# Kernel tuning notes

Hardware: AMD Instinct MI355X
Metric: run time of the kernel (lower is better)

The kernel has to match this reference:

```python
import jax, jax.numpy as jnp
import numpy as np

N = 100000

def _gcn_norm(edge_index, n):
    # PyG GCNConv default: add self-loops, symmetric deg^-1/2 normalization
    loops = jnp.arange(n, dtype=edge_index.dtype)
    src = jnp.concatenate([edge_index[0], loops])
    dst = jnp.concatenate([edge_index[1], loops])
    deg = jax.ops.segment_sum(jnp.ones_like(dst, dtype=jnp.float32), dst, num_segments=n)
    dinv = jnp.where(deg > 0, jax.lax.rsqrt(deg), 0.0)
    norm = dinv[src] * dinv[dst]  # [E+N]
    return src, dst, norm

def _gcn_conv(h, W, b, src, dst, norm, n):
    # transform then gather-scale-scatter aggregate
    h = h @ W                                   # [N, out]
    out = jax.ops.segment_sum(norm[:, None] * h[src], dst, num_segments=n)
    return out + b

def _prelu(h, a):
    return jnp.where(h > 0, h, a * h)

def _dropout(h, u, p=0.5):
    # deterministic dropout: keep where u >= p, scale by 1/(1-p)
    return jnp.where(u >= p, h / (1.0 - p), 0.0)

def setup_inputs() -> dict:
    key = jax.random.key(0)
    ks = jax.random.split(key, 12)
    D, H1, H2, C, E = 512, 128, 16, 10, 1600000
    x = jax.random.normal(ks[0], (N, D), dtype=jnp.float32)
    edge_index = jax.random.randint(ks[1], (2, E), 0, N, dtype=jnp.int64)
    u1 = jax.random.uniform(ks[2], (N, H1), dtype=jnp.float32)
    u2 = jax.random.uniform(ks[3], (N, H2), dtype=jnp.float32)
    def glorot(k, shp):
        lim = np.sqrt(6.0 / (shp[0] + shp[1]))
        return jax.random.uniform(k, shp, dtype=jnp.float32, minval=-lim, maxval=lim)
    W1 = glorot(ks[4], (D, H1)); b1 = jnp.zeros((H1,), jnp.float32)
    W2 = glorot(ks[5], (H1, H2)); b2 = jnp.zeros((H2,), jnp.float32)
    fcW = glorot(ks[6], (H2, C)); fcb = jnp.zeros((C,), jnp.float32)
    a = jnp.float32(0.25)  # PReLU init (shared single param for both layers)
    return {"x": x, "edge_index": edge_index, "W1": W1, "b1": b1, "W2": W2,
            "b2": b2, "a": a, "fcW": fcW, "fcb": fcb, "u1": u1, "u2": u2}

def reference(x, edge_index, W1, b1, W2, b2, a, fcW, fcb, u1, u2):
    src, dst, norm = _gcn_norm(edge_index, N)
    feat1 = _dropout(_prelu(_gcn_conv(x, W1, b1, src, dst, norm, N), a), u1)
    feat2 = _dropout(_prelu(_gcn_conv(feat1, W2, b2, src, dst, norm, N), a), u2)
    logits = feat2 @ fcW + fcb
    return (feat2, logits)
```

## Files before the change

### kernel.cpp

```cpp
#include <hip/hip_runtime.h>
#include <hip/hip_bf16.h>
#include <stdint.h>

#define NN 100000
#define DIN 512
#define H1C 128
#define H2C 16
#define NCLS 10
#define NB_SCAN ((NN + 255) / 256)

typedef __attribute__((ext_vector_type(8))) short s16x8;
typedef __attribute__((ext_vector_type(4))) float f32x4;
typedef __attribute__((ext_vector_type(4))) unsigned short u16x4;
typedef __attribute__((ext_vector_type(8))) unsigned short u16x8;

static __device__ __forceinline__ unsigned short f2bf(float f) {
  __hip_bfloat16 h = __float2bfloat16(f);
  return *(unsigned short*)&h;
}
static __device__ __forceinline__ float bflo(unsigned u) {
  return __uint_as_float(u << 16);
}
static __device__ __forceinline__ float bfhi(unsigned u) {
  return __uint_as_float(u & 0xffff0000u);
}

__device__ __forceinline__ int ld_src(const int* __restrict__ ei, int f, int E, int i) {
  return f ? ei[2 * (size_t)i] : ei[i];
}
__device__ __forceinline__ int ld_dst(const int* __restrict__ ei, int f, int E, int i) {
  return f ? ei[2 * ((size_t)E + (size_t)i)] : ei[(size_t)E + (size_t)i];
}

__global__ void k_pre(const int* __restrict__ ei, int* __restrict__ flag,
                      int* __restrict__ deg,
                      const float* __restrict__ W1, unsigned short* __restrict__ Wt, int n) {
  int i = blockIdx.x * 256 + threadIdx.x;
  if (blockIdx.x == 0 && threadIdx.x < 64) {
    int v = ei[2 * threadIdx.x + 1];
    unsigned long long b = __ballot(v == 0);
    if (threadIdx.x == 0) *flag = (b == ~0ull) ? 1 : 0;
  }
  if (i < n) deg[i] = 0;
  if (i < H1C * DIN) {
    int nn = i >> 9, k = i & 511;
    Wt[i] = f2bf(W1[(size_t)k * H1C + nn]);
  }
}

__global__ void k_count(const int* __restrict__ ei, const int* __restrict__ flag,
                        int E, int* __restrict__ deg, int* __restrict__ rank) {
  int i = blockIdx.x * blockDim.x + threadIdx.x;
  if (i >= E) return;
  int f = *flag;
  rank[i] = atomicAdd(&deg[ld_dst(ei, f, E, i)], 1);
}

__global__ void k_scanA(const int* __restrict__ deg, int* __restrict__ incl,
                        int* __restrict__ bsum, float* __restrict__ dinv, int n) {
  __shared__ int s[256];
  int i = blockIdx.x * 256 + threadIdx.x;
  int v = (i < n) ? deg[i] : 0;
  if (i < n) dinv[i] = rsqrtf((float)(v + 1));
  s[threadIdx.x] = v;
  __syncthreads();
  for (int off = 1; off < 256; off <<= 1) {
    int t = (threadIdx.x >= off) ? s[threadIdx.x - off] : 0;
    __syncthreads();
    s[threadIdx.x] += t;
    __syncthreads();
  }
  if (i < n) incl[i] = s[threadIdx.x];
  if (threadIdx.x == 255) bsum[blockIdx.x] = s[255];
}

__global__ void k_scanB(int* __restrict__ bsum, int nb) {
  __shared__ int s[512];
  int v = (threadIdx.x < nb) ? bsum[threadIdx.x] : 0;
  s[threadIdx.x] = v;
  __syncthreads();
  for (int off = 1; off < 512; off <<= 1) {
    int t = (threadIdx.x >= off) ? s[threadIdx.x - off] : 0;
    __syncthreads();
    s[threadIdx.x] += t;
    __syncthreads();
  }
  if (threadIdx.x < nb) bsum[threadIdx.x] = s[threadIdx.x] - v;
}

__global__ void k_scanC(const int* __restrict__ deg, const int* __restrict__ bsum,
                        int* __restrict__ offs, int n, int E) {
  int i = blockIdx.x * 256 + threadIdx.x;
  if (i < n) offs[i] = offs[i] - deg[i] + bsum[i >> 8];
  if (i == 0) offs[n] = E;
}

__global__ void k_scatter(const int* __restrict__ ei, const int* __restrict__ flag, int E,
                          const int* __restrict__ offs, const int* __restrict__ rank,
                          const float* __restrict__ dinv, uint2* __restrict__ csr_sw) {
  int i = blockIdx.x * blockDim.x + threadIdx.x;
  if (i >= E) return;
  int f = *flag;
  int s = ld_src(ei, f, E, i), d = ld_dst(ei, f, E, i);
  int pos = offs[d] + rank[i];
  uint2 rec;
  rec.x = (unsigned)s;
  rec.y = __float_as_uint(dinv[s]);
  csr_sw[pos] = rec;
}

#define BM 128
#define BK 64
#define LDA 72
#define LDB 72

__global__ __launch_bounds__(256) void k_gemm1_mfma(const float* __restrict__ x,
                                                    const unsigned short* __restrict__ Wt,
                                                    unsigned int* __restrict__ h1u, int n) {
  __shared__ unsigned short As[BM * LDA];
  __shared__ unsigned short Bs[H1C * LDB];
  int tid = threadIdx.x;
  int wave = tid >> 6, lane = tid & 63;
  int wm = wave >> 1, wn = wave & 1;
  int bm = blockIdx.x * BM;
  int lrow = lane & 15, lk = (lane >> 4) * 8;

  f32x4 acc[4][4];
#pragma unroll
  for (int i = 0; i < 4; i++)
#pragma unroll
    for (int j = 0; j < 4; j++) acc[i][j] = (f32x4){0.f, 0.f, 0.f, 0.f};

  for (int k0 = 0; k0 < DIN; k0 += BK) {
#pragma unroll
    for (int p = 0; p < 8; p++) {
      int idx = p * 256 + tid;
      int r = idx >> 4, c4 = (idx & 15) * 4;
      int row = bm + r;
      float4 v = make_float4(0.f, 0.f, 0.f, 0.f);
      if (row < n) v = *(const float4*)(x + (size_t)row * DIN + k0 + c4);
      u16x4 b4;
      b4.x = f2bf(v.x); b4.y = f2bf(v.y); b4.z = f2bf(v.z); b4.w = f2bf(v.w);
      *(u16x4*)&As[r * LDA + c4] = b4;
    }
#pragma unroll
    for (int p = 0; p < 4; p++) {
      int idx = p * 256 + tid;
      int r = idx >> 3, c8 = (idx & 7) * 8;
      int pr = (r & 64) + (((r & 1) + 2 * ((r >> 5) & 1)) << 4) + ((r >> 1) & 15);
      u16x8 v = *(const u16x8*)&Wt[(size_t)r * DIN + k0 + c8];
      *(u16x8*)&Bs[pr * LDB + c8] = v;
    }
    __syncthreads();
#pragma unroll
    for (int kk = 0; kk < 2; kk++) {
      s16x8 a[4], b[4];
#pragma unroll
      for (int mi = 0; mi < 4; mi++)
        a[mi] = *(const s16x8*)&As[(wm * 64 + mi * 16 + lrow) * LDA + kk * 32 + lk];
#pragma unroll
      for (int nj = 0; nj < 4; nj++)
        b[nj] = *(const s16x8*)&Bs[(wn * 64 + nj * 16 + lrow) * LDB + kk * 32 + lk];
#pragma unroll
      for (int mi = 0; mi < 4; mi++)
#pragma unroll
        for (int nj = 0; nj < 4; nj++)
          acc[mi][nj] = __builtin_amdgcn_mfma_f32_16x16x32_bf16(a[mi], b[nj], acc[mi][nj], 0, 0, 0);
    }
    __syncthreads();
  }
#pragma unroll
  for (int mi = 0; mi < 4; mi++) {
#pragma unroll
    for (int r = 0; r < 4; r++) {
      int row = bm + wm * 64 + mi * 16 + (lane >> 4) * 4 + r;
      if (row < n) {
        unsigned p0 = ((unsigned)f2bf(acc[mi][1][r]) << 16) | (unsigned)f2bf(acc[mi][0][r]);
        unsigned p1 = ((unsigned)f2bf(acc[mi][3][r]) << 16) | (unsigned)f2bf(acc[mi][2][r]);
        h1u[(size_t)row * 64 + wn * 32 + lrow] = p0;
        h1u[(size_t)row * 64 + wn * 32 + 16 + lrow] = p1;
      }
    }
  }
}

__global__ __launch_bounds__(256) void k_agg1(const unsigned int* __restrict__ h1u,
                                              const uint2* __restrict__ csr_sw,
                                              const int* __restrict__ offs,
                                              const float* __restrict__ dinv,
                                              const float* __restrict__ b1,
                                              const float* __restrict__ aP,
                                              const float* __restrict__ u1,
                                              unsigned int* __restrict__ f1u, int n) {
  int wid = (blockIdx.x * 256 + threadIdx.x) >> 6;
  int lane = threadIdx.x & 63;
  if (wid >= n) return;
  int d = wid;
  int beg = offs[d], end = offs[d + 1];
  unsigned gs = h1u[(size_t)d * 64 + lane];
  float ax = 0.f, ay = 0.f;
  int e = beg;
  for (; e + 7 < end; e += 8) {
    uint2 r0 = csr_sw[e],     r1 = csr_sw[e + 1], r2 = csr_sw[e + 2], r3 = csr_sw[e + 3];
    uint2 r4 = csr_sw[e + 4], r5 = csr_sw[e + 5], r6 = csr_sw[e + 6], r7 = csr_sw[e + 7];
    unsigned g0 = h1u[(size_t)r0.x * 64 + lane];
    unsigned g1 = h1u[(size_t)r1.x * 64 + lane];
    unsigned g2 = h1u[(size_t)r2.x * 64 + lane];
    unsigned g3 = h1u[(size_t)r3.x * 64 + lane];
    unsigned g4 = h1u[(size_t)r4.x * 64 + lane];
    unsigned g5 = h1u[(size_t)r5.x * 64 + lane];
    unsigned g6 = h1u[(size_t)r6.x * 64 + lane];
    unsigned g7 = h1u[(size_t)r7.x * 64 + lane];
    float w0 = __uint_as_float(r0.y), w1 = __uint_as_float(r1.y);
    float w2 = __uint_as_float(r2.y), w3 = __uint_as_float(r3.y);
    float w4 = __uint_as_float(r4.y), w5 = __uint_as_float(r5.y);
    float w6 = __uint_as_float(r6.y), w7 = __uint_as_float(r7.y);
    ax += w0 * bflo(g0); ay += w0 * bfhi(g0);
    ax += w1 * bflo(g1); ay += w1 * bfhi(g1);
    ax += w2 * bflo(g2); ay += w2 * bfhi(g2);
    ax += w3 * bflo(g3); ay += w3 * bfhi(g3);
    ax += w4 * bflo(g4); ay += w4 * bfhi(g4);
    ax += w5 * bflo(g5); ay += w5 * bfhi(g5);
    ax += w6 * bflo(g6); ay += w6 * bfhi(g6);
    ax += w7 * bflo(g7); ay += w7 * bfhi(g7);
  }
  for (; e + 3 < end; e += 4) {
    uint2 r0 = csr_sw[e], r1 = csr_sw[e + 1], r2 = csr_sw[e + 2], r3 = csr_sw[e + 3];
    unsigned g0 = h1u[(size_t)r0.x * 64 + lane];
    unsigned g1 = h1u[(size_t)r1.x * 64 + lane];
    unsigned g2 = h1u[(size_t)r2.x * 64 + lane];
    unsigned g3 = h1u[(size_t)r3.x * 64 + lane];
    float w0 = __uint_as_float(r0.y), w1 = __uint_as_float(r1.y);
    float w2 = __uint_as_float(r2.y), w3 = __uint_as_float(r3.y);
    ax += w0 * bflo(g0); ay += w0 * bfhi(g0);
    ax += w1 * bflo(g1); ay += w1 * bfhi(g1);
    ax += w2 * bflo(g2); ay += w2 * bfhi(g2);
    ax += w3 * bflo(g3); ay += w3 * bfhi(g3);
  }
  for (; e < end; e++) {
    uint2 rr = csr_sw[e];
    float w = __uint_as_float(rr.y);
    unsigned g = h1u[(size_t)rr.x * 64 + lane];
    ax += w * bflo(g); ay += w * bfhi(g);
  }
  float di = dinv[d];
  ax = (ax + di * bflo(gs)) * di;
  ay = (ay + di * bfhi(gs)) * di;
  float2 bb = ((const float2*)b1)[lane];
  ax += bb.x; ay += bb.y;
  float al = *aP;
  ax = ax > 0.f ? ax : al * ax;
  ay = ay > 0.f ? ay : al * ay;
  float2 uu = ((const float2*)u1)[(size_t)d * 64 + lane];
  ax = (uu.x >= 0.5f) ? ax * 2.f : 0.f;
  ay = (uu.y >= 0.5f) ? ay * 2.f : 0.f;
  unsigned pk = ((unsigned)f2bf(ay) << 16) | (unsigned)f2bf(ax);
  f1u[(size_t)d * 64 + lane] = pk;
}

__global__ __launch_bounds__(256) void k_gemm2(const unsigned int* __restrict__ f1u,
                                               const float* __restrict__ W2,
                                               unsigned int* __restrict__ h2u, int n) {
  __shared__ float ws[H1C][H2C];
  __shared__ unsigned int fs[16][66];
  int tid = threadIdx.x;
#pragma unroll
  for (int p = 0; p < 8; p++) {
    int idx = tid + p * 256;
    ws[idx >> 4][idx & 15] = W2[idx];
  }
  int r0 = blockIdx.x * 16;
  {
    int r = tid >> 4, c4 = (tid & 15) * 4;
    int row = r0 + r;
    uint4 v = make_uint4(0, 0, 0, 0);
    if (row < n) v = *(const uint4*)(f1u + (size_t)row * 64 + c4);
    *(uint4*)&fs[r][c4] = v;
  }
  __syncthreads();
  int col = tid & 15, r = tid >> 4;
  float acc = 0.f;
#pragma unroll
  for (int k = 0; k < 64; k++) {
    unsigned u = fs[r][k];
    acc += bflo(u) * ws[2 * k][col] + bfhi(u) * ws[2 * k + 1][col];
  }
  int row = r0 + r;
  float accN = __shfl_xor(acc, 1, 64);
  if ((col & 1) == 0 && row < n) {
    unsigned pk = ((unsigned)f2bf(accN) << 16) | (unsigned)f2bf(acc);
    h2u[(size_t)row * 8 + (col >> 1)] = pk;
  }
}

__global__ __launch_bounds__(256) void k_agg2(const unsigned int* __restrict__ h2u,
                                              const uint2* __restrict__ csr_sw,
                                              const int* __restrict__ offs,
                                              const float* __restrict__ dinv,
                                              const float* __restrict__ b2,
                                              const float* __restrict__ aP,
                                              const float* __restrict__ u2,
                                              const float* __restrict__ fcW,
                                              const float* __restrict__ fcb,
                                              float* __restrict__ out_feat2,
                                              float* __restrict__ out_logits, int n) {
  int wid = (blockIdx.x * 256 + threadIdx.x) >> 6;
  int lane = threadIdx.x & 63;
  if (wid >= n) return;
  int d = wid;
  int g = lane >> 3, j = lane & 7;
  int beg = offs[d], end = offs[d + 1];
  unsigned gs = h2u[(size_t)d * 8 + j];
  float aa = 0.f, ab = 0.f;
  int e = beg + g;
  for (; e + 8 < end; e += 16) {
    uint2 r0 = csr_sw[e], r1 = csr_sw[e + 8];
    unsigned g0 = h2u[(size_t)r0.x * 8 + j];
    unsigned g1 = h2u[(size_t)r1.x * 8 + j];
    float w0 = __uint_as_float(r0.y), w1 = __uint_as_float(r1.y);
    aa += w0 * bflo(g0) + w1 * bflo(g1);
    ab += w0 * bfhi(g0) + w1 * bfhi(g1);
  }
  for (; e < end; e += 8) {
    uint2 rr = csr_sw[e];
    unsigned gg = h2u[(size_t)rr.x * 8 + j];
    float w = __uint_as_float(rr.y);
    aa += w * bflo(gg); ab += w * bfhi(gg);
  }
  aa += __shfl_xor(aa, 8, 64); aa += __shfl_xor(aa, 16, 64); aa += __shfl_xor(aa, 32, 64);
  ab += __shfl_xor(ab, 8, 64); ab += __shfl_xor(ab, 16, 64); ab += __shfl_xor(ab, 32, 64);
  float di = dinv[d];
  aa = (aa + di * bflo(gs)) * di;
  ab = (ab + di * bfhi(gs)) * di;
  aa += b2[2 * j]; ab += b2[2 * j + 1];
  float al = *aP;
  aa = aa > 0.f ? aa : al * aa;
  ab = ab > 0.f ? ab : al * ab;
  float2 uu = ((const float2*)(u2 + (size_t)d * H2C))[j];
  aa = (uu.x >= 0.5f) ? aa * 2.f : 0.f;
  ab = (uu.y >= 0.5f) ? ab * 2.f : 0.f;
  if (lane < 8) {
    float2 o; o.x = aa; o.y = ab;
    ((float2*)(out_feat2 + (size_t)d * H2C))[j] = o;
  }
  int c = lane & 15;
  int cc = (c < NCLS) ? c : 0;
  float lg = fcb[cc];
#pragma unroll
  for (int k = 0; k < 8; k++) {
    float va = __shfl(aa, k, 64);
    float vb = __shfl(ab, k, 64);
    lg += va * fcW[(2 * k) * NCLS + cc] + vb * fcW[(2 * k + 1) * NCLS + cc];
  }
  if (lane < NCLS) out_logits[(size_t)d * NCLS + c] = lg;
}

extern "C" void kernel_launch(void* const* d_in, const int* in_sizes, int n_in,
                              void* d_out, int out_size, void* d_ws, size_t ws_size,
                              hipStream_t stream) {
  const float* x   = (const float*)d_in[0];
  const int*   ei  = (const int*)d_in[1];
  const float* W1  = (const float*)d_in[2];
  const float* b1  = (const float*)d_in[3];
  const float* W2  = (const float*)d_in[4];
  const float* b2  = (const float*)d_in[5];
  const float* aP  = (const float*)d_in[6];
  const float* fcW = (const float*)d_in[7];
  const float* fcb = (const float*)d_in[8];
  const float* u1  = (const float*)d_in[9];
  const float* u2  = (const float*)d_in[10];
  const int E = in_sizes[1] / 2;

  float* out_feat2  = (float*)d_out;
  float* out_logits = (float*)d_out + (size_t)NN * H2C;

  char* w = (char*)d_ws;
  size_t off = 0;
  auto A = [&](size_t bytes) -> char* {
    char* p = w + off;
    off = (off + bytes + 255) & ~(size_t)255;
    return p;
  };
  int*   flag   = (int*)A(256);
  int*   deg    = (int*)A((size_t)NN * 4);
  int*   offs   = (int*)A((size_t)(NN + 1) * 4);
  float* dinv   = (float*)A((size_t)NN * 4);
  int*   bsum   = (int*)A(512 * 4);
  int*   rank   = (int*)A((size_t)E * 4);
  uint2* csr_sw = (uint2*)A((size_t)E * 8);
  unsigned int* h1u = (unsigned int*)A((size_t)NN * 64 * 4);
  unsigned int* f1u = (unsigned int*)A((size_t)NN * 64 * 4);
  unsigned int* h2u = (unsigned int*)A((size_t)NN * 8 * 4);
  unsigned short* Wt = (unsigned short*)A((size_t)H1C * DIN * 2);

  dim3 b256(256);
  int gE = (E + 255) / 256;
  int gN = (NN + 255) / 256;

  k_pre<<<gN, b256, 0, stream>>>(ei, flag, deg, W1, Wt, NN);
  k_count<<<gE, b256, 0, stream>>>(ei, flag, E, deg, rank);
  k_scanA<<<NB_SCAN, b256, 0, stream>>>(deg, offs, bsum, dinv, NN);
  k_scanB<<<1, 512, 0, stream>>>(bsum, NB_SCAN);
  k_scanC<<<gN, b256, 0, stream>>>(deg, bsum, offs, NN, E);
  k_scatter<<<gE, b256, 0, stream>>>(ei, flag, E, offs, rank, dinv, csr_sw);
  k_gemm1_mfma<<<(NN + BM - 1) / BM, b256, 0, stream>>>(x, Wt, h1u, NN);
  k_agg1<<<(NN + 3) / 4, b256, 0, stream>>>(h1u, csr_sw, offs, dinv, b1, aP, u1, f1u, NN);
  k_gemm2<<<(NN + 15) / 16, b256, 0, stream>>>(f1u, W2, h2u, NN);
  k_agg2<<<(NN + 3) / 4, b256, 0, stream>>>(h2u, csr_sw, offs, dinv, b2, aP, u2,
                                            fcW, fcb, out_feat2, out_logits, NN);
}
```

Before: 370.7 us.

## Halve GEMM1 row tile and prefetch next K-slice into registers

The first-layer GEMM now uses 64-row tiles instead of 128, which doubles the block count and shrinks the accumulator arrays. It also adds register double-buffering: global loads for the next K-slice are issued before the MFMA compute on the current shared-memory tile, so load latency can overlap with compute. The cost is more blocks, which re-read W1 more often, and extra registers for the prefetch buffers.

```diff
diff --git a/kernel.cpp b/kernel.cpp
--- a/kernel.cpp
+++ b/kernel.cpp
@@ -109,7 +109,7 @@
   csr_sw[pos] = rec;
 }
 
-#define BM 128
+#define BM 64
 #define BK 64
 #define LDA 72
 #define LDB 72
@@ -125,44 +125,66 @@
   int bm = blockIdx.x * BM;
   int lrow = lane & 15, lk = (lane >> 4) * 8;
 
-  f32x4 acc[4][4];
-#pragma unroll
-  for (int i = 0; i < 4; i++)
+  f32x4 acc[2][4];
+#pragma unroll
+  for (int i = 0; i < 2; i++)
 #pragma unroll
     for (int j = 0; j < 4; j++) acc[i][j] = (f32x4){0.f, 0.f, 0.f, 0.f};
 
-  for (int k0 = 0; k0 < DIN; k0 += BK) {
-#pragma unroll
-    for (int p = 0; p < 8; p++) {
+  float4 areg[4];
+  u16x8 breg[4];
+
+  auto loadA = [&](int k0) {
+#pragma unroll
+    for (int p = 0; p < 4; p++) {
       int idx = p * 256 + tid;
       int r = idx >> 4, c4 = (idx & 15) * 4;
       int row = bm + r;
-      float4 v = make_float4(0.f, 0.f, 0.f, 0.f);
-      if (row < n) v = *(const float4*)(x + (size_t)row * DIN + k0 + c4);
-      u16x4 b4;
-      b4.x = f2bf(v.x); b4.y = f2bf(v.y); b4.z = f2bf(v.z); b4.w = f2bf(v.w);
-      *(u16x4*)&As[r * LDA + c4] = b4;
-    }
+      areg[p] = make_float4(0.f, 0.f, 0.f, 0.f);
+      if (row < n) areg[p] = *(const float4*)(x + (size_t)row * DIN + k0 + c4);
+    }
+  };
+  auto loadB = [&](int k0) {
 #pragma unroll
     for (int p = 0; p < 4; p++) {
       int idx = p * 256 + tid;
       int r = idx >> 3, c8 = (idx & 7) * 8;
-      int pr = (r & 64) + (((r & 1) + 2 * ((r >> 5) & 1)) << 4) + ((r >> 1) & 15);
-      u16x8 v = *(const u16x8*)&Wt[(size_t)r * DIN + k0 + c8];
-      *(u16x8*)&Bs[pr * LDB + c8] = v;
+      breg[p] = *(const u16x8*)&Wt[(size_t)r * DIN + k0 + c8];
+    }
+  };
+
+  loadA(0);
+  loadB(0);
+
+  for (int k0 = 0; k0 < DIN; k0 += BK) {
+#pragma unroll
+    for (int p = 0; p < 4; p++) {
+      int idx = p * 256 + tid;
+      int r = idx >> 4, c4 = (idx & 15) * 4;
+      u16x4 b4;
+      b4.x = f2bf(areg[p].x); b4.y = f2bf(areg[p].y);
+      b4.z = f2bf(areg[p].z); b4.w = f2bf(areg[p].w);
+      *(u16x4*)&As[r * LDA + c4] = b4;
+      int rb = idx >> 3, c8 = (idx & 7) * 8;
+      int pr = (rb & 64) + (((rb & 1) + 2 * ((rb >> 5) & 1)) << 4) + ((rb >> 1) & 15);
+      *(u16x8*)&Bs[pr * LDB + c8] = breg[p];
+    }
+    if (k0 + BK < DIN) {
+      loadA(k0 + BK);
+      loadB(k0 + BK);
     }
     __syncthreads();
 #pragma unroll
     for (int kk = 0; kk < 2; kk++) {
-      s16x8 a[4], b[4];
-#pragma unroll
-      for (int mi = 0; mi < 4; mi++)
-        a[mi] = *(const s16x8*)&As[(wm * 64 + mi * 16 + lrow) * LDA + kk * 32 + lk];
+      s16x8 a[2], b[4];
+#pragma unroll
+      for (int mi = 0; mi < 2; mi++)
+        a[mi] = *(const s16x8*)&As[(wm * 32 + mi * 16 + lrow) * LDA + kk * 32 + lk];
 #pragma unroll
       for (int nj = 0; nj < 4; nj++)
         b[nj] = *(const s16x8*)&Bs[(wn * 64 + nj * 16 + lrow) * LDB + kk * 32 + lk];
 #pragma unroll
-      for (int mi = 0; mi < 4; mi++)
+      for (int mi = 0; mi < 2; mi++)
 #pragma unroll
         for (int nj = 0; nj < 4; nj++)
           acc[mi][nj] = __builtin_amdgcn_mfma_f32_16x16x32_bf16(a[mi], b[nj], acc[mi][nj], 0, 0, 0);
@@ -170,10 +192,10 @@
     __syncthreads();
   }
 #pragma unroll
-  for (int mi = 0; mi < 4; mi++) {
+  for (int mi = 0; mi < 2; mi++) {
 #pragma unroll
     for (int r = 0; r < 4; r++) {
-      int row = bm + wm * 64 + mi * 16 + (lane >> 4) * 4 + r;
+      int row = bm + wm * 32 + mi * 16 + (lane >> 4) * 4 + r;
       if (row < n) {
         unsigned p0 = ((unsigned)f2bf(acc[mi][1][r]) << 16) | (unsigned)f2bf(acc[mi][0][r]);
         unsigned p1 = ((unsigned)f2bf(acc[mi][3][r]) << 16) | (unsigned)f2bf(acc[mi][2][r]);
```

Measured after the change: 325.0 us. 12.3% less time.
